# Optimization experiments

Measured on AMD Instinct MI355X. Metric: run time of the kernel, lower is better.

Reference implementation:

```python
import jax, jax.numpy as jnp
import numpy as np

INPUT_DIM = 1024
HIDDEN = 1024
MASKED = INPUT_DIM // 2  # even indices are the conditioning half
BATCH = 65536


def setup_inputs() -> dict:
    key = jax.random.key(0)
    ks = jax.random.split(key, 7)
    s1 = 1.0 / np.sqrt(MASKED)
    s2 = 1.0 / np.sqrt(HIDDEN)
    x = jax.random.normal(ks[0], (BATCH, INPUT_DIM), dtype=jnp.float32)
    W1 = jax.random.uniform(ks[1], (MASKED, HIDDEN), jnp.float32, -s1, s1)
    b1 = jax.random.uniform(ks[2], (HIDDEN,), jnp.float32, -s1, s1)
    W2 = jax.random.uniform(ks[3], (HIDDEN, HIDDEN), jnp.float32, -s2, s2)
    b2 = jax.random.uniform(ks[4], (HIDDEN,), jnp.float32, -s2, s2)
    W3 = jax.random.uniform(ks[5], (HIDDEN, INPUT_DIM - MASKED), jnp.float32, -s2, s2)
    b3 = jax.random.uniform(ks[6], (INPUT_DIM - MASKED,), jnp.float32, -s2, s2)
    return {"x": x, "W1": W1, "b1": b1, "W2": W2, "b2": b2, "W3": W3, "b3": b3}


def reference(x, W1, b1, W2, b2, W3, b3):
    # mask_type='even': mask[::2]=1 -> even indices conditioning, odd indices translated
    masked = x[:, 0::2]  # [B, MASKED], gather of conditioning half
    h = jax.nn.relu(masked @ W1 + b1)
    h = jax.nn.relu(h @ W2 + b2)
    translation = h @ W3 + b3  # [B, INPUT_DIM - MASKED]
    # scatter-add translation into odd positions
    y = x.at[:, 1::2].add(translation)
    return y
```

## Files before the change

kernel.cpp:

```cpp
#include <hip/hip_runtime.h>
#include <stdint.h>

#define BATCH  65536
#define IN_DIM 1024
#define MASKED 512
#define HIDDEN 1024

typedef unsigned short u16;
typedef __bf16 bf16x8 __attribute__((ext_vector_type(8)));
typedef float  f32x4  __attribute__((ext_vector_type(4)));

typedef __attribute__((address_space(1))) void gvoid;
typedef __attribute__((address_space(3))) void lvoid;

__device__ __forceinline__ u16 f32_to_bf16(float f) {
    union { float f; uint32_t u; } v; v.f = f;
    uint32_t r = v.u + 0x7FFFu + ((v.u >> 16) & 1u);
    return (u16)(r >> 16);
}

__global__ void prep_xm(const float* __restrict__ x, u16* __restrict__ xm) {
    int idx = blockIdx.x * blockDim.x + threadIdx.x;
    const float4* xv = reinterpret_cast<const float4*>(x);
    float4 v0 = xv[idx * 2];
    float4 v1 = xv[idx * 2 + 1];
    ushort4 o;
    o.x = f32_to_bf16(v0.x);
    o.y = f32_to_bf16(v0.z);
    o.z = f32_to_bf16(v1.x);
    o.w = f32_to_bf16(v1.z);
    reinterpret_cast<ushort4*>(xm)[idx] = o;
}

__global__ void wconv(const float* __restrict__ W, u16* __restrict__ Wt,
                      int K, int N) {
    __shared__ float t[32][33];
    const int nbk = K / 32;
    const int bk = blockIdx.x % nbk;
    const int bn = blockIdx.x / nbk;
    const int tx = threadIdx.x & 31;
    const int ty = threadIdx.x >> 5;
    const int k0 = bk * 32, n0 = bn * 32;
    #pragma unroll
    for (int i = 0; i < 4; ++i)
        t[ty + i * 8][tx] = W[(int64_t)(k0 + ty + i * 8) * N + n0 + tx];
    __syncthreads();
    #pragma unroll
    for (int i = 0; i < 4; ++i)
        Wt[(int64_t)(n0 + ty + i * 8) * K + k0 + tx] = f32_to_bf16(t[tx][ty + i * 8]);
}

template<int K, int N, int MODE>
__global__ __launch_bounds__(256, 3)
void gemm_bt(const u16* __restrict__ A, const u16* __restrict__ Bt,
             const float* __restrict__ bias,
             u16* __restrict__ Cb,
             const float* __restrict__ X,
             float* __restrict__ Y) {
    constexpr int BK = 64;
    __shared__ u16 As[128 * BK];
    __shared__ u16 Bs[128 * BK];

    const int tid  = threadIdx.x;
    const int lane = tid & 63;
    const int w    = tid >> 6;
    const int wr   = w >> 1;
    const int wc   = w & 1;

    constexpr int nbn = N / 128;
    const int bm = blockIdx.x / nbn;
    const int bn = blockIdx.x % nbn;
    const int m0 = bm * 128;
    const int n0 = bn * 128;

    f32x4 acc[4][4];
    #pragma unroll
    for (int i = 0; i < 4; ++i)
        #pragma unroll
        for (int j = 0; j < 4; ++j)
            acc[i][j] = f32x4{0.f, 0.f, 0.f, 0.f};

    const int srow = lane >> 3;
    const int scol = (lane & 7) * 8;
    const u16* aptr = A  + (int64_t)(m0 + w * 32 + srow) * K + scol;
    const u16* bptr = Bt + (int64_t)(n0 + w * 32 + srow) * K + scol;

    for (int kt = 0; kt < K / BK; ++kt) {
        __syncthreads();
        const int koff = kt * BK;
        #pragma unroll
        for (int c = 0; c < 4; ++c) {
            __builtin_amdgcn_global_load_lds(
                (gvoid*)(aptr + koff + c * 8 * K),
                (lvoid*)(&As[(w * 32 + c * 8) * BK]), 16, 0, 0);
            __builtin_amdgcn_global_load_lds(
                (gvoid*)(bptr + koff + c * 8 * K),
                (lvoid*)(&Bs[(w * 32 + c * 8) * BK]), 16, 0, 0);
        }
        __syncthreads();

        #pragma unroll
        for (int kk = 0; kk < 2; ++kk) {
            bf16x8 a[4], b[4];
            #pragma unroll
            for (int i = 0; i < 4; ++i)
                a[i] = *reinterpret_cast<const bf16x8*>(
                    &As[(wr * 64 + i * 16 + (lane & 15)) * BK + kk * 32 + (lane >> 4) * 8]);
            #pragma unroll
            for (int j = 0; j < 4; ++j)
                b[j] = *reinterpret_cast<const bf16x8*>(
                    &Bs[(wc * 64 + j * 16 + (lane & 15)) * BK + kk * 32 + (lane >> 4) * 8]);
            #pragma unroll
            for (int i = 0; i < 4; ++i)
                #pragma unroll
                for (int j = 0; j < 4; ++j)
                    acc[i][j] = __builtin_amdgcn_mfma_f32_16x16x32_bf16(
                        a[i], b[j], acc[i][j], 0, 0, 0);
        }
    }

    const int cl = lane & 15;
    const int rg = (lane >> 4) * 4;
    #pragma unroll
    for (int j = 0; j < 4; ++j) {
        const int n  = n0 + wc * 64 + j * 16 + cl;
        const float bv = bias[n];
        #pragma unroll
        for (int i = 0; i < 4; ++i) {
            #pragma unroll
            for (int r = 0; r < 4; ++r) {
                const int m = m0 + wr * 64 + i * 16 + rg + r;
                float v = acc[i][j][r] + bv;
                if (MODE == 0) {
                    v = v > 0.f ? v : 0.f;
                    Cb[(int64_t)m * N + n] = f32_to_bf16(v);
                } else {
                    const int64_t p = (int64_t)m * IN_DIM + 2 * n;
                    float2 xv = *reinterpret_cast<const float2*>(&X[p]);
                    float2 o;
                    o.x = xv.x;
                    o.y = xv.y + v;
                    *reinterpret_cast<float2*>(&Y[p]) = o;
                }
            }
        }
    }
}

extern "C" void kernel_launch(void* const* d_in, const int* in_sizes, int n_in,
                              void* d_out, int out_size, void* d_ws, size_t ws_size,
                              hipStream_t stream) {
    const float* x  = (const float*)d_in[0];
    const float* W1 = (const float*)d_in[1];
    const float* b1 = (const float*)d_in[2];
    const float* W2 = (const float*)d_in[3];
    const float* b2 = (const float*)d_in[4];
    const float* W3 = (const float*)d_in[5];
    const float* b3 = (const float*)d_in[6];
    float* y = (float*)d_out;

    char* ws = (char*)d_ws;
    u16* h1  = (u16*)(ws);
    u16* h2  = (u16*)(ws + 134217728);
    u16* xm  = (u16*)(ws + 134217728);
    u16* W1t = (u16*)(ws + 268435456);
    u16* W2t = (u16*)(ws + 268435456 + 1048576);
    u16* W3t = (u16*)(ws + 268435456 + 1048576 + 2097152);

    prep_xm<<<BATCH * IN_DIM / 8 / 256, 256, 0, stream>>>(x, xm);

    wconv<<<(MASKED / 32) * (HIDDEN / 32), 256, 0, stream>>>(W1, W1t, MASKED, HIDDEN);
    wconv<<<(HIDDEN / 32) * (HIDDEN / 32), 256, 0, stream>>>(W2, W2t, HIDDEN, HIDDEN);
    wconv<<<(HIDDEN / 32) * ((IN_DIM - MASKED) / 32), 256, 0, stream>>>(W3, W3t, HIDDEN, IN_DIM - MASKED);

    gemm_bt<MASKED, HIDDEN, 0><<<(BATCH / 128) * (HIDDEN / 128), 256, 0, stream>>>(
        xm, W1t, b1, h1, nullptr, nullptr);
    gemm_bt<HIDDEN, HIDDEN, 0><<<(BATCH / 128) * (HIDDEN / 128), 256, 0, stream>>>(
        h1, W2t, b2, h2, nullptr, nullptr);
    gemm_bt<HIDDEN, IN_DIM - MASKED, 1><<<(BATCH / 128) * ((IN_DIM - MASKED) / 128), 256, 0, stream>>>(
        h2, W3t, b3, nullptr, x, y);
}
```

Baseline: 514.8 us.

## Fuse three MLP GEMMs into one kernel keeping activations in LDS

Replaces the three separate bf16 GEMM launches with one kernel. Each 512-thread block owns 64 batch rows and keeps the layer-1 chunk and the full layer-2 output in shared memory, with swizzled layouts. Weight tiles stream through a triple-buffered async global-to-LDS pipeline with manual waitcnt, barriers and setprio. This removes the global round-trips of the h1/h2 intermediates, which are large at batch 65536. The cost is one block per CU with about 152 KB of LDS and a heavy register footprint from the full layer-2 accumulators, and every block re-reads all the weights.

```diff
diff --git a/kernel.cpp b/kernel.cpp
--- a/kernel.cpp
+++ b/kernel.cpp
@@ -12,6 +12,10 @@
 
 typedef __attribute__((address_space(1))) void gvoid;
 typedef __attribute__((address_space(3))) void lvoid;
+
+#define WAITV(N) asm volatile("s_waitcnt vmcnt(" #N ")" ::: "memory")
+#define WAITL0() asm volatile("s_waitcnt lgkmcnt(0)" ::: "memory")
+#define FENCE()  asm volatile("" ::: "memory")
 
 __device__ __forceinline__ u16 f32_to_bf16(float f) {
     union { float f; uint32_t u; } v; v.f = f;
@@ -50,101 +54,264 @@
         Wt[(int64_t)(n0 + ty + i * 8) * K + k0 + tx] = f32_to_bf16(t[tx][ty + i * 8]);
 }
 
-template<int K, int N, int MODE>
-__global__ __launch_bounds__(256, 3)
-void gemm_bt(const u16* __restrict__ A, const u16* __restrict__ Bt,
-             const float* __restrict__ bias,
-             u16* __restrict__ Cb,
-             const float* __restrict__ X,
-             float* __restrict__ Y) {
-    constexpr int BK = 64;
-    __shared__ u16 As[128 * BK];
-    __shared__ u16 Bs[128 * BK];
+__global__ __launch_bounds__(512, 1)
+void mlp_fused(const u16* __restrict__ xm,
+               const u16* __restrict__ W1t, const u16* __restrict__ W2t,
+               const u16* __restrict__ W3t,
+               const float* __restrict__ b1, const float* __restrict__ b2,
+               const float* __restrict__ b3,
+               const float* __restrict__ X, float* __restrict__ Y) {
+    __shared__ __align__(16) char pool[155648];
+    u16* const XM = (u16*)pool;
+    u16* const HQ = (u16*)(pool + 114688);
+    u16* const H2 = (u16*)pool;
 
     const int tid  = threadIdx.x;
     const int lane = tid & 63;
     const int w    = tid >> 6;
-    const int wr   = w >> 1;
-    const int wc   = w & 1;
-
-    constexpr int nbn = N / 128;
-    const int bm = blockIdx.x / nbn;
-    const int bn = blockIdx.x % nbn;
-    const int m0 = bm * 128;
-    const int n0 = bn * 128;
-
-    f32x4 acc[4][4];
-    #pragma unroll
-    for (int i = 0; i < 4; ++i)
-        #pragma unroll
-        for (int j = 0; j < 4; ++j)
-            acc[i][j] = f32x4{0.f, 0.f, 0.f, 0.f};
-
-    const int srow = lane >> 3;
-    const int scol = (lane & 7) * 8;
-    const u16* aptr = A  + (int64_t)(m0 + w * 32 + srow) * K + scol;
-    const u16* bptr = Bt + (int64_t)(n0 + w * 32 + srow) * K + scol;
-
-    for (int kt = 0; kt < K / BK; ++kt) {
-        __syncthreads();
-        const int koff = kt * BK;
-        #pragma unroll
-        for (int c = 0; c < 4; ++c) {
-            __builtin_amdgcn_global_load_lds(
-                (gvoid*)(aptr + koff + c * 8 * K),
-                (lvoid*)(&As[(w * 32 + c * 8) * BK]), 16, 0, 0);
-            __builtin_amdgcn_global_load_lds(
-                (gvoid*)(bptr + koff + c * 8 * K),
-                (lvoid*)(&Bs[(w * 32 + c * 8) * BK]), 16, 0, 0);
+    const int m0   = blockIdx.x * 64;
+
+    const int cl    = lane & 15;
+    const int rg    = (lane >> 4) * 4;
+    const int klane = lane >> 4;
+    const int sw7   = lane & 7;
+
+    const int wm3 = w >> 2, wn3 = w & 3;
+
+    auto stage12 = [&](int pp) {
+        char* dstb = pool + 65536 + (pp % 3) * 16384;
+        const int q2 = pp / 48;
+        const int r2 = pp - q2 * 48;
+        #pragma unroll
+        for (int i = 0; i < 2; ++i) {
+            const int c = i * 512 + tid;
+            const int srow = c >> 2;
+            const int scs  = ((c & 3) ^ ((srow + (srow >> 2)) & 3)) * 8;
+            const u16* g;
+            if (r2 < 16) {
+                g = W1t + (q2 * 256 + srow) * 512 + r2 * 32 + scs;
+            } else {
+                const int rr2 = r2 - 16;
+                g = W2t + ((rr2 >> 3) * 256 + srow) * 1024 + q2 * 256 + (rr2 & 7) * 32 + scs;
+            }
+            __builtin_amdgcn_global_load_lds((gvoid*)g, (lvoid*)(dstb + c * 16), 16, 0, 0);
         }
-        __syncthreads();
-
-        #pragma unroll
-        for (int kk = 0; kk < 2; ++kk) {
-            bf16x8 a[4], b[4];
-            #pragma unroll
-            for (int i = 0; i < 4; ++i)
-                a[i] = *reinterpret_cast<const bf16x8*>(
-                    &As[(wr * 64 + i * 16 + (lane & 15)) * BK + kk * 32 + (lane >> 4) * 8]);
-            #pragma unroll
-            for (int j = 0; j < 4; ++j)
-                b[j] = *reinterpret_cast<const bf16x8*>(
-                    &Bs[(wc * 64 + j * 16 + (lane & 15)) * BK + kk * 32 + (lane >> 4) * 8]);
-            #pragma unroll
-            for (int i = 0; i < 4; ++i)
-                #pragma unroll
-                for (int j = 0; j < 4; ++j)
-                    acc[i][j] = __builtin_amdgcn_mfma_f32_16x16x32_bf16(
-                        a[i], b[j], acc[i][j], 0, 0, 0);
+    };
+    auto stage3 = [&](int pp) {
+        char* dstb = pool + 131072 + (pp % 3) * 8192;
+        const int c = tid;
+        const int srow = c >> 2;
+        const int scs  = ((c & 3) ^ ((srow + (srow >> 2)) & 3)) * 8;
+        const u16* g = W3t + ((pp >> 5) * 128 + srow) * 1024 + (pp & 31) * 32 + scs;
+        __builtin_amdgcn_global_load_lds((gvoid*)g, (lvoid*)(dstb + c * 16), 16, 0, 0);
+    };
+
+    float b1v[4][2];
+    #pragma unroll
+    for (int i = 0; i < 4; ++i)
+        #pragma unroll
+        for (int nf = 0; nf < 2; ++nf)
+            b1v[i][nf] = b1[i * 256 + w * 32 + nf * 16 + cl];
+
+    #pragma unroll
+    for (int i = 0; i < 8; ++i) {
+        const int c = i * 512 + tid;
+        const int row = c >> 6, cc = c & 63;
+        const u16* g = xm + (int64_t)(m0 + row) * 512 + ((cc ^ (row & 7)) * 8);
+        __builtin_amdgcn_global_load_lds((gvoid*)g, (lvoid*)(pool + c * 16), 16, 0, 0);
+    }
+    stage12(0); stage12(1);
+    WAITV(2);
+    __builtin_amdgcn_s_barrier(); FENCE();
+
+    f32x4 acc2[4][4][2];
+    #pragma unroll
+    for (int a = 0; a < 4; ++a)
+        #pragma unroll
+        for (int b = 0; b < 4; ++b)
+            #pragma unroll
+            for (int c = 0; c < 2; ++c)
+                acc2[a][b][c] = f32x4{0.f, 0.f, 0.f, 0.f};
+
+    #pragma unroll
+    for (int q = 0; q < 4; ++q) {
+        f32x4 acc1[4][2];
+        #pragma unroll
+        for (int a = 0; a < 4; ++a)
+            #pragma unroll
+            for (int b = 0; b < 2; ++b)
+                acc1[a][b] = f32x4{0.f, 0.f, 0.f, 0.f};
+
+        for (int r = 0; r < 16; ++r) {
+            const int p = q * 48 + r;
+            const u16* sl = (const u16*)(pool + 65536 + (p % 3) * 16384);
+            bf16x8 a[4], bb[2];
+            #pragma unroll
+            for (int mf = 0; mf < 4; ++mf)
+                a[mf] = *(const bf16x8*)(XM + (cl + mf * 16) * 512 +
+                                         (((r * 4 + klane) ^ sw7) * 8));
+            #pragma unroll
+            for (int nf = 0; nf < 2; ++nf) {
+                const int row = w * 32 + nf * 16 + cl;
+                bb[nf] = *(const bf16x8*)(sl + row * 32 +
+                                          ((klane ^ ((row + (row >> 2)) & 3)) * 8));
+            }
+            if (p + 2 < 192) stage12(p + 2);
+            __builtin_amdgcn_s_setprio(1);
+            #pragma unroll
+            for (int mf = 0; mf < 4; ++mf)
+                #pragma unroll
+                for (int nf = 0; nf < 2; ++nf)
+                    acc1[mf][nf] = __builtin_amdgcn_mfma_f32_16x16x32_bf16(
+                        a[mf], bb[nf], acc1[mf][nf], 0, 0, 0);
+            __builtin_amdgcn_s_setprio(0);
+            WAITL0(); __builtin_amdgcn_sched_barrier(0);
+            if (p + 2 < 192) { WAITV(2); } else { WAITV(0); }
+            __builtin_amdgcn_s_barrier(); FENCE();
+        }
+
+        #pragma unroll
+        for (int mf = 0; mf < 4; ++mf)
+            #pragma unroll
+            for (int nf = 0; nf < 2; ++nf) {
+                const int nq = w * 32 + nf * 16 + cl;
+                #pragma unroll
+                for (int rr = 0; rr < 4; ++rr) {
+                    const int m = mf * 16 + rg + rr;
+                    float v = acc1[mf][nf][rr] + b1v[q][nf];
+                    v = v > 0.f ? v : 0.f;
+                    HQ[m * 256 + (((nq >> 3) ^ (m & 7)) * 8 + (nq & 7))] = f32_to_bf16(v);
+                }
+            }
+        WAITL0();
+        __builtin_amdgcn_s_barrier(); FENCE();
+
+        #pragma unroll
+        for (int nc = 0; nc < 4; ++nc) {
+            for (int kt2 = 0; kt2 < 8; ++kt2) {
+                const int p = q * 48 + 16 + nc * 8 + kt2;
+                const u16* sl = (const u16*)(pool + 65536 + (p % 3) * 16384);
+                bf16x8 a[4], bb[2];
+                #pragma unroll
+                for (int mf = 0; mf < 4; ++mf)
+                    a[mf] = *(const bf16x8*)(HQ + (cl + mf * 16) * 256 +
+                                             (((kt2 * 4 + klane) ^ sw7) * 8));
+                #pragma unroll
+                for (int nf = 0; nf < 2; ++nf) {
+                    const int row = w * 32 + nf * 16 + cl;
+                    bb[nf] = *(const bf16x8*)(sl + row * 32 +
+                                              ((klane ^ ((row + (row >> 2)) & 3)) * 8));
+                }
+                if (p + 2 < 192) stage12(p + 2);
+                __builtin_amdgcn_s_setprio(1);
+                #pragma unroll
+                for (int mf = 0; mf < 4; ++mf)
+                    #pragma unroll
+                    for (int nf = 0; nf < 2; ++nf)
+                        acc2[nc][mf][nf] = __builtin_amdgcn_mfma_f32_16x16x32_bf16(
+                            a[mf], bb[nf], acc2[nc][mf][nf], 0, 0, 0);
+                __builtin_amdgcn_s_setprio(0);
+                WAITL0(); __builtin_amdgcn_sched_barrier(0);
+                if (p + 2 < 192) { WAITV(2); } else { WAITV(0); }
+                __builtin_amdgcn_s_barrier(); FENCE();
+            }
         }
     }
 
-    const int cl = lane & 15;
-    const int rg = (lane >> 4) * 4;
-    #pragma unroll
-    for (int j = 0; j < 4; ++j) {
-        const int n  = n0 + wc * 64 + j * 16 + cl;
-        const float bv = bias[n];
-        #pragma unroll
-        for (int i = 0; i < 4; ++i) {
-            #pragma unroll
-            for (int r = 0; r < 4; ++r) {
-                const int m = m0 + wr * 64 + i * 16 + rg + r;
-                float v = acc[i][j][r] + bv;
-                if (MODE == 0) {
+    float b2v[4][2];
+    #pragma unroll
+    for (int i = 0; i < 4; ++i)
+        #pragma unroll
+        for (int nf = 0; nf < 2; ++nf)
+            b2v[i][nf] = b2[i * 256 + w * 32 + nf * 16 + cl];
+    WAITV(0);
+    #pragma unroll
+    for (int nc = 0; nc < 4; ++nc)
+        #pragma unroll
+        for (int mf = 0; mf < 4; ++mf)
+            #pragma unroll
+            for (int nf = 0; nf < 2; ++nf) {
+                const int n2 = nc * 256 + w * 32 + nf * 16 + cl;
+                #pragma unroll
+                for (int rr = 0; rr < 4; ++rr) {
+                    const int m = mf * 16 + rg + rr;
+                    float v = acc2[nc][mf][nf][rr] + b2v[nc][nf];
                     v = v > 0.f ? v : 0.f;
-                    Cb[(int64_t)m * N + n] = f32_to_bf16(v);
-                } else {
+                    H2[m * 1024 + (((n2 >> 3) ^ (m & 7)) * 8 + (n2 & 7))] = f32_to_bf16(v);
+                }
+            }
+    WAITL0();
+    __builtin_amdgcn_s_barrier(); FENCE();
+
+    float b3v[4][2];
+    #pragma unroll
+    for (int i = 0; i < 4; ++i)
+        #pragma unroll
+        for (int nf = 0; nf < 2; ++nf)
+            b3v[i][nf] = b3[i * 128 + wn3 * 32 + nf * 16 + cl];
+    stage3(0); stage3(1);
+    WAITV(1);
+    __builtin_amdgcn_s_barrier(); FENCE();
+
+    f32x4 acc3[4][2][2];
+    #pragma unroll
+    for (int a = 0; a < 4; ++a)
+        #pragma unroll
+        for (int b = 0; b < 2; ++b)
+            #pragma unroll
+            for (int c = 0; c < 2; ++c)
+                acc3[a][b][c] = f32x4{0.f, 0.f, 0.f, 0.f};
+
+    #pragma unroll
+    for (int nc3 = 0; nc3 < 4; ++nc3) {
+        for (int kt3 = 0; kt3 < 32; ++kt3) {
+            const int p3 = nc3 * 32 + kt3;
+            const u16* sl3 = (const u16*)(pool + 131072 + (p3 % 3) * 8192);
+            bf16x8 a3[2], bf3[2];
+            #pragma unroll
+            for (int mf = 0; mf < 2; ++mf)
+                a3[mf] = *(const bf16x8*)(H2 + (wm3 * 32 + cl + mf * 16) * 1024 +
+                                          (((kt3 * 4 + klane) ^ sw7) * 8));
+            #pragma unroll
+            for (int nf = 0; nf < 2; ++nf) {
+                const int row = wn3 * 32 + nf * 16 + cl;
+                bf3[nf] = *(const bf16x8*)(sl3 + row * 32 +
+                                           ((klane ^ ((row + (row >> 2)) & 3)) * 8));
+            }
+            if (p3 + 2 < 128) stage3(p3 + 2);
+            __builtin_amdgcn_s_setprio(1);
+            #pragma unroll
+            for (int mf = 0; mf < 2; ++mf)
+                #pragma unroll
+                for (int nf = 0; nf < 2; ++nf)
+                    acc3[nc3][mf][nf] = __builtin_amdgcn_mfma_f32_16x16x32_bf16(
+                        a3[mf], bf3[nf], acc3[nc3][mf][nf], 0, 0, 0);
+            __builtin_amdgcn_s_setprio(0);
+            WAITL0(); __builtin_amdgcn_sched_barrier(0);
+            if (p3 + 2 < 128) { WAITV(1); } else { WAITV(0); }
+            __builtin_amdgcn_s_barrier(); FENCE();
+        }
+    }
+
+    #pragma unroll
+    for (int nc3 = 0; nc3 < 4; ++nc3)
+        #pragma unroll
+        for (int mf = 0; mf < 2; ++mf)
+            #pragma unroll
+            for (int nf = 0; nf < 2; ++nf) {
+                const int n = nc3 * 128 + wn3 * 32 + nf * 16 + cl;
+                #pragma unroll
+                for (int rr = 0; rr < 4; ++rr) {
+                    const int m = m0 + wm3 * 32 + mf * 16 + rg + rr;
+                    const float t = acc3[nc3][mf][nf][rr] + b3v[nc3][nf];
                     const int64_t p = (int64_t)m * IN_DIM + 2 * n;
                     float2 xv = *reinterpret_cast<const float2*>(&X[p]);
                     float2 o;
                     o.x = xv.x;
-                    o.y = xv.y + v;
+                    o.y = xv.y + t;
                     *reinterpret_cast<float2*>(&Y[p]) = o;
                 }
             }
-        }
-    }
 }
 
 extern "C" void kernel_launch(void* const* d_in, const int* in_sizes, int n_in,
@@ -160,12 +327,10 @@
     float* y = (float*)d_out;
 
     char* ws = (char*)d_ws;
-    u16* h1  = (u16*)(ws);
-    u16* h2  = (u16*)(ws + 134217728);
-    u16* xm  = (u16*)(ws + 134217728);
-    u16* W1t = (u16*)(ws + 268435456);
-    u16* W2t = (u16*)(ws + 268435456 + 1048576);
-    u16* W3t = (u16*)(ws + 268435456 + 1048576 + 2097152);
+    u16* xm  = (u16*)(ws);
+    u16* W1t = (u16*)(ws + 67108864);
+    u16* W2t = (u16*)(ws + 67108864 + 1048576);
+    u16* W3t = (u16*)(ws + 67108864 + 1048576 + 2097152);
 
     prep_xm<<<BATCH * IN_DIM / 8 / 256, 256, 0, stream>>>(x, xm);
 
@@ -173,10 +338,5 @@
     wconv<<<(HIDDEN / 32) * (HIDDEN / 32), 256, 0, stream>>>(W2, W2t, HIDDEN, HIDDEN);
     wconv<<<(HIDDEN / 32) * ((IN_DIM - MASKED) / 32), 256, 0, stream>>>(W3, W3t, HIDDEN, IN_DIM - MASKED);
 
-    gemm_bt<MASKED, HIDDEN, 0><<<(BATCH / 128) * (HIDDEN / 128), 256, 0, stream>>>(
-        xm, W1t, b1, h1, nullptr, nullptr);
-    gemm_bt<HIDDEN, HIDDEN, 0><<<(BATCH / 128) * (HIDDEN / 128), 256, 0, stream>>>(
-        h1, W2t, b2, h2, nullptr, nullptr);
-    gemm_bt<HIDDEN, IN_DIM - MASKED, 1><<<(BATCH / 128) * ((IN_DIM - MASKED) / 128), 256, 0, stream>>>(
-        h2, W3t, b3, nullptr, x, y);
-}
+    mlp_fused<<<BATCH / 64, 512, 0, stream>>>(xm, W1t, W2t, W3t, b1, b2, b3, x, y);
+}
```

New measurement: 601.5 us. 1.17x slower.
